# Kernel optimization log

Measured on AMD Instinct MI355X. Metric: run time of the kernel, lower is better.

Reference implementation:

```python
import jax, jax.numpy as jnp
import numpy as np

N = 8192
IN_F = 512
OUT_F = 64
ALPHA = 0.2   # LeakyReLU negative slope
STDV = 0.2
NEG_INF = -9e15


def setup_inputs() -> dict:
    key = jax.random.key(0)
    k1, k2, k3, k4 = jax.random.split(key, 4)
    x = jax.random.normal(k1, (N, IN_F), dtype=jnp.float32)
    adj = jax.random.randint(k2, (N, N), 0, 2, dtype=jnp.int32)
    W = jax.random.normal(k3, (IN_F, OUT_F), dtype=jnp.float32) * STDV
    a = jax.random.normal(k4, (2 * OUT_F, 1), dtype=jnp.float32) * STDV
    return {"x": x, "adj": adj, "W": W, "a": a}


def reference(x, adj, W, a):
    # Wh: [N, F']
    Wh = x @ W
    # attention logits: e[i,j] = leakyrelu(Wh[i]@a1 + Wh[j]@a2)
    Wh1 = Wh @ a[:OUT_F, :]   # [N, 1]
    Wh2 = Wh @ a[OUT_F:, :]   # [N, 1]
    e = Wh1 + Wh2.T           # [N, N] via broadcast
    e = jnp.where(e >= 0, e, ALPHA * e)  # LeakyReLU
    # mask by adjacency, row softmax
    masked = jnp.where(adj > 0, e, jnp.float32(NEG_INF))
    attention = jax.nn.softmax(masked, axis=1)
    # dropout rate is 0.0 in this config -> identity
    h_prime = attention @ Wh  # [N, F']
    out = jnp.where(h_prime > 0, h_prime, jnp.expm1(h_prime))  # ELU
    return out, attention
```

## Files before the change

kernel.cpp:

```cpp
#include <hip/hip_runtime.h>
#include <cmath>

#define Nn    8192
#define INF_  512
#define OUTF  64

typedef __attribute__((ext_vector_type(4))) int   i4;
typedef __attribute__((ext_vector_type(4))) float f4v;
typedef __attribute__((ext_vector_type(8))) short s8;
typedef __attribute__((ext_vector_type(4))) float f32x4;
typedef unsigned long long u64;

__device__ __forceinline__ float lrelu(float v) { return fmaxf(v, 0.2f * v); }

__device__ __forceinline__ unsigned int f2bf(float f) {
    unsigned int u = __float_as_uint(f);
    u = (u + 0x7FFFu + ((u >> 16) & 1u)) >> 16;
    return u;
}

__global__ __launch_bounds__(1024, 8) void k1_wh(
    const float* __restrict__ x, const float* __restrict__ W,
    const float* __restrict__ a, unsigned short* __restrict__ WhT,
    float* __restrict__ Wh1, float* __restrict__ Wh2)
{
    __shared__ float part[3][16][64];
    __shared__ unsigned short stage[64][16];
    const int t    = threadIdx.x;
    const int s    = t >> 8;
    const int r    = (t >> 4) & 15;
    const int cg   = (t & 15) << 2;
    const int row0 = blockIdx.x * 16;
    const int row  = row0 + r;
    const float* __restrict__ xr = x + (size_t)row * INF_ + s * 128;
    const float* __restrict__ Wp = W + (size_t)s * 128 * OUTF;

    float4 acc = make_float4(0.f, 0.f, 0.f, 0.f);
    for (int k = 0; k < 128; k += 4) {
        const float4 xv = *(const float4*)(xr + k);
        const float* wp = Wp + (size_t)k * OUTF + cg;
        const float4 w0 = *(const float4*)(wp);
        const float4 w1 = *(const float4*)(wp + OUTF);
        const float4 w2 = *(const float4*)(wp + 2 * OUTF);
        const float4 w3 = *(const float4*)(wp + 3 * OUTF);
        acc.x += xv.x * w0.x + xv.y * w1.x + xv.z * w2.x + xv.w * w3.x;
        acc.y += xv.x * w0.y + xv.y * w1.y + xv.z * w2.y + xv.w * w3.y;
        acc.z += xv.x * w0.z + xv.y * w1.z + xv.z * w2.z + xv.w * w3.z;
        acc.w += xv.x * w0.w + xv.y * w1.w + xv.z * w2.w + xv.w * w3.w;
    }
    if (s > 0) *(float4*)&part[s - 1][r][cg] = acc;
    __syncthreads();
    if (s == 0) {
        const float4 pa = *(const float4*)&part[0][r][cg];
        const float4 pb = *(const float4*)&part[1][r][cg];
        const float4 pc = *(const float4*)&part[2][r][cg];
        acc.x += pa.x + pb.x + pc.x;
        acc.y += pa.y + pb.y + pc.y;
        acc.z += pa.z + pb.z + pc.z;
        acc.w += pa.w + pb.w + pc.w;
        stage[cg + 0][r] = (unsigned short)f2bf(acc.x);
        stage[cg + 1][r] = (unsigned short)f2bf(acc.y);
        stage[cg + 2][r] = (unsigned short)f2bf(acc.z);
        stage[cg + 3][r] = (unsigned short)f2bf(acc.w);

        float p1 = acc.x * a[cg]        + acc.y * a[cg + 1]
                 + acc.z * a[cg + 2]    + acc.w * a[cg + 3];
        float p2 = acc.x * a[OUTF + cg]     + acc.y * a[OUTF + cg + 1]
                 + acc.z * a[OUTF + cg + 2] + acc.w * a[OUTF + cg + 3];
        #pragma unroll
        for (int off = 8; off; off >>= 1) {
            p1 += __shfl_xor(p1, off);
            p2 += __shfl_xor(p2, off);
        }
        if ((t & 15) == 0) { Wh1[row] = p1; Wh2[row] = p2; }
    }
    __syncthreads();
    if (t < 256) {
        const int col = t >> 2;
        const int q   = t & 3;
        const u64 v = *(const u64*)&stage[col][q * 4];
        *(u64*)(WhT + (size_t)col * Nn + row0 + q * 4) = v;
    }
}

__global__ __launch_bounds__(1024, 8) void k2_fused(
    const int* __restrict__ adj, const unsigned short* __restrict__ WhT,
    const float* __restrict__ Wh1, const float* __restrict__ Wh2,
    float* __restrict__ outp, float* __restrict__ att)
{
    __shared__ alignas(16) unsigned short att_t[2][16 * 256];
    __shared__ float red[3][4][16][16];

    const int t    = threadIdx.x;
    const int lane = t & 63;
    const int w    = t >> 6;
    const int row0 = blockIdx.x * 16;
    const int row  = row0 + w;
    const int* __restrict__ adjrow = adj + (size_t)row * Nn;
    const float h1 = Wh1[row];

    u64 mk0 = 0, mk1 = 0;
    float S = 0.f;
    {
        i4 av[4];
        #pragma unroll
        for (int i = 0; i < 4; ++i)
            av[i] = *((const i4*)(adjrow + 256 * i) + lane);
        #pragma unroll
        for (int i = 0; i < 32; ++i) {
            const i4 a = av[i & 3];
            if (i < 28)
                av[i & 3] = *((const i4*)(adjrow + 256 * (i + 4)) + lane);
            const f4v w4 = *((const f4v*)(Wh2 + 256 * i) + lane);
            const int nib = (a.x != 0 ? 1 : 0) | (a.y != 0 ? 2 : 0)
                          | (a.z != 0 ? 4 : 0) | (a.w != 0 ? 8 : 0);
            S += (nib & 1) ? __expf(lrelu(h1 + w4.x)) : 0.f;
            S += (nib & 2) ? __expf(lrelu(h1 + w4.y)) : 0.f;
            S += (nib & 4) ? __expf(lrelu(h1 + w4.z)) : 0.f;
            S += (nib & 8) ? __expf(lrelu(h1 + w4.w)) : 0.f;
            if (i < 16) mk0 |= (u64)nib << (i * 4);
            else        mk1 |= (u64)nib << ((i - 16) * 4);
        }
    }
    #pragma unroll
    for (int off = 32; off; off >>= 1) S += __shfl_xor(S, off);
    const float is = 1.0f / S;

    const int ct = w & 3;
    const int kq = w >> 2;
    f32x4 acc = {0.f, 0.f, 0.f, 0.f};

    auto produce = [&](int c, int bf) {
        const int jb = c * 256;
        const f4v w2 = *((const f4v*)(Wh2 + jb) + lane);
        const int nib = (int)(((c & 16) ? mk1 : mk0) >> ((c & 15) * 4)) & 15;
        const float v0 = (nib & 1) ? __expf(lrelu(h1 + w2.x)) * is : 0.f;
        const float v1 = (nib & 2) ? __expf(lrelu(h1 + w2.y)) * is : 0.f;
        const float v2 = (nib & 4) ? __expf(lrelu(h1 + w2.z)) * is : 0.f;
        const float v3 = (nib & 8) ? __expf(lrelu(h1 + w2.w)) * is : 0.f;
        f4v st; st.x = v0; st.y = v1; st.z = v2; st.w = v3;
        __builtin_nontemporal_store(st, (f4v*)(att + (size_t)row * Nn + jb) + lane);
        const u64 pk = (u64)(f2bf(v0) | (f2bf(v1) << 16))
                     | ((u64)(f2bf(v2) | (f2bf(v3) << 16)) << 32);
        int byte = w * 512 + lane * 8;  byte ^= (w & 7) << 4;
        *(u64*)((char*)att_t[bf] + byte) = pk;
    };

    const int ar = lane & 15;
    const int ag = lane >> 4;
    auto bload = [&](int c, int ss) -> s8 {
        const int ks = kq * 2 + ss;
        return *(const s8*)(WhT + (size_t)(ct * 16 + ar) * Nn
                            + c * 256 + ks * 32 + ag * 8);
    };
    auto amfma = [&](int bf, s8 b0, s8 b1) {
        #pragma unroll
        for (int ss = 0; ss < 2; ++ss) {
            const int ks = kq * 2 + ss;
            int byte = ar * 512 + ks * 64 + ag * 16;
            byte ^= (ar & 7) << 4;
            const s8 af = *(const s8*)((char*)att_t[bf] + byte);
            acc = __builtin_amdgcn_mfma_f32_16x16x32_bf16(af, ss ? b1 : b0, acc, 0, 0, 0);
        }
    };

    s8 b0 = bload(0, 0), b1 = bload(0, 1);
    produce(0, 0);
    asm volatile("s_waitcnt lgkmcnt(0)" ::: "memory");
    __builtin_amdgcn_s_barrier();
    for (int c = 0; c < Nn / 256 - 1; ++c) {
        produce(c + 1, (c + 1) & 1);
        const s8 nb0 = bload(c + 1, 0);
        const s8 nb1 = bload(c + 1, 1);
        amfma(c & 1, b0, b1);
        asm volatile("s_waitcnt lgkmcnt(0)" ::: "memory");
        __builtin_amdgcn_s_barrier();
        b0 = nb0; b1 = nb1;
    }
    amfma((Nn / 256 - 1) & 1, b0, b1);

    __syncthreads();
    if (kq > 0) {
        #pragma unroll
        for (int q = 0; q < 4; ++q) red[kq - 1][ct][ag * 4 + q][ar] = acc[q];
    }
    __syncthreads();
    if (kq == 0) {
        #pragma unroll
        for (int q = 0; q < 4; ++q) {
            const int r = ag * 4 + q;
            float v = acc[q] + red[0][ct][r][ar] + red[1][ct][r][ar] + red[2][ct][r][ar];
            v = v > 0.f ? v : expm1f(v);
            outp[(size_t)(row0 + r) * OUTF + ct * 16 + ar] = v;
        }
    }
}

extern "C" void kernel_launch(void* const* d_in, const int* in_sizes, int n_in,
                              void* d_out, int out_size, void* d_ws, size_t ws_size,
                              hipStream_t stream)
{
    const float* x   = (const float*)d_in[0];
    const int*   adj = (const int*)d_in[1];
    const float* W   = (const float*)d_in[2];
    const float* a   = (const float*)d_in[3];

    float* outp = (float*)d_out;
    float* att  = outp + (size_t)Nn * OUTF;

    float* Wh1 = (float*)d_ws;
    float* Wh2 = Wh1 + Nn;
    unsigned short* WhT = (unsigned short*)(Wh2 + Nn);

    hipLaunchKernelGGL(k1_wh,    dim3(Nn / 16), dim3(1024), 0, stream,
                       x, W, a, WhT, Wh1, Wh2);
    hipLaunchKernelGGL(k2_fused, dim3(Nn / 16), dim3(1024), 0, stream,
                       adj, WhT, Wh1, Wh2, outp, att);
}
```

Before: 179.0 us.

## Stage x tile in LDS and block-cooperatively stream adjacency into shared bitmask

In k1, the 16x512 x tile is loaded cooperatively into shared memory with nontemporal loads, and the GEMV reads x from LDS instead of per-thread global reads. In k2, the whole block streams 16 adjacency rows contiguously (each thread covers 4 columns across all rows) instead of one wave per row. Neighbor masks go into an 8-bit-per-nibble LDS bitmask, and the per-row softmax denominators are reduced across waves through shared memory. The aim is more coalesced, longer streaming access to the dominant 256MB adj read. The cost is extra LDS (32KB bitmask), extra barriers, and a one-ahead prefetch instead of four.

Measured after the change: 162.0 us. -9.5%, faster.

```diff
diff --git a/kernel.cpp b/kernel.cpp
--- a/kernel.cpp
+++ b/kernel.cpp
@@ -24,20 +24,30 @@
     const float* __restrict__ a, unsigned short* __restrict__ WhT,
     float* __restrict__ Wh1, float* __restrict__ Wh2)
 {
+    __shared__ float xs[16][520];
     __shared__ float part[3][16][64];
     __shared__ unsigned short stage[64][16];
     const int t    = threadIdx.x;
+    const int row0 = blockIdx.x * 16;
+
+    #pragma unroll
+    for (int s2 = 0; s2 < 2; ++s2) {
+        const int idx = s2 * 4096 + 4 * t;
+        const f4v v = __builtin_nontemporal_load(
+            (const f4v*)(x + (size_t)row0 * INF_ + idx));
+        *(f4v*)&xs[idx >> 9][idx & 511] = v;
+    }
+    __syncthreads();
+
     const int s    = t >> 8;
     const int r    = (t >> 4) & 15;
     const int cg   = (t & 15) << 2;
-    const int row0 = blockIdx.x * 16;
     const int row  = row0 + r;
-    const float* __restrict__ xr = x + (size_t)row * INF_ + s * 128;
     const float* __restrict__ Wp = W + (size_t)s * 128 * OUTF;
 
     float4 acc = make_float4(0.f, 0.f, 0.f, 0.f);
     for (int k = 0; k < 128; k += 4) {
-        const float4 xv = *(const float4*)(xr + k);
+        const float4 xv = *(const float4*)&xs[r][s * 128 + k];
         const float* wp = Wp + (size_t)k * OUTF + cg;
         const float4 w0 = *(const float4*)(wp);
         const float4 w1 = *(const float4*)(wp + OUTF);
@@ -88,43 +98,61 @@
     const float* __restrict__ Wh1, const float* __restrict__ Wh2,
     float* __restrict__ outp, float* __restrict__ att)
 {
+    __shared__ unsigned char bm8[16][2048];
     __shared__ alignas(16) unsigned short att_t[2][16 * 256];
     __shared__ float red[3][4][16][16];
+    __shared__ float sm_Sp[16][16];
+    __shared__ float sm_is[16];
 
     const int t    = threadIdx.x;
     const int lane = t & 63;
     const int w    = t >> 6;
     const int row0 = blockIdx.x * 16;
-    const int row  = row0 + w;
-    const int* __restrict__ adjrow = adj + (size_t)row * Nn;
+
+    {
+        const i4* __restrict__ asrc = (const i4*)(adj + (size_t)row0 * Nn);
+        const int j0 = 4 * t;
+        const f4v w4a = *(const f4v*)(Wh2 + j0);
+        const f4v w4b = *(const f4v*)(Wh2 + 4096 + j0);
+        float Sp = 0.f;
+        i4 av = __builtin_nontemporal_load(asrc + t);
+        #pragma unroll
+        for (int s = 0; s < 32; ++s) {
+            const int r = s >> 1, h = s & 1;
+            i4 nxt;
+            if (s < 31)
+                nxt = __builtin_nontemporal_load(asrc + (s + 1) * 1024 + t);
+            const f4v w4 = h ? w4b : w4a;
+            const float h1r = Wh1[row0 + r];
+            const int nib = (av.x != 0 ? 1 : 0) | (av.y != 0 ? 2 : 0)
+                          | (av.z != 0 ? 4 : 0) | (av.w != 0 ? 8 : 0);
+            Sp += (nib & 1) ? __expf(lrelu(h1r + w4.x)) : 0.f;
+            Sp += (nib & 2) ? __expf(lrelu(h1r + w4.y)) : 0.f;
+            Sp += (nib & 4) ? __expf(lrelu(h1r + w4.z)) : 0.f;
+            Sp += (nib & 8) ? __expf(lrelu(h1r + w4.w)) : 0.f;
+            bm8[r][h * 1024 + t] = (unsigned char)nib;
+            if (h) {
+                #pragma unroll
+                for (int off = 32; off; off >>= 1) Sp += __shfl_xor(Sp, off);
+                if (lane == 0) sm_Sp[r][w] = Sp;
+                Sp = 0.f;
+            }
+            av = nxt;
+        }
+    }
+    __syncthreads();
+
+    {
+        float sv = sm_Sp[w][lane & 15];
+        #pragma unroll
+        for (int off = 8; off; off >>= 1) sv += __shfl_xor(sv, off);
+        if (lane == 0) sm_is[w] = 1.0f / sv;
+    }
+    __syncthreads();
+
+    const int row = row0 + w;
     const float h1 = Wh1[row];
-
-    u64 mk0 = 0, mk1 = 0;
-    float S = 0.f;
-    {
-        i4 av[4];
-        #pragma unroll
-        for (int i = 0; i < 4; ++i)
-            av[i] = *((const i4*)(adjrow + 256 * i) + lane);
-        #pragma unroll
-        for (int i = 0; i < 32; ++i) {
-            const i4 a = av[i & 3];
-            if (i < 28)
-                av[i & 3] = *((const i4*)(adjrow + 256 * (i + 4)) + lane);
-            const f4v w4 = *((const f4v*)(Wh2 + 256 * i) + lane);
-            const int nib = (a.x != 0 ? 1 : 0) | (a.y != 0 ? 2 : 0)
-                          | (a.z != 0 ? 4 : 0) | (a.w != 0 ? 8 : 0);
-            S += (nib & 1) ? __expf(lrelu(h1 + w4.x)) : 0.f;
-            S += (nib & 2) ? __expf(lrelu(h1 + w4.y)) : 0.f;
-            S += (nib & 4) ? __expf(lrelu(h1 + w4.z)) : 0.f;
-            S += (nib & 8) ? __expf(lrelu(h1 + w4.w)) : 0.f;
-            if (i < 16) mk0 |= (u64)nib << (i * 4);
-            else        mk1 |= (u64)nib << ((i - 16) * 4);
-        }
-    }
-    #pragma unroll
-    for (int off = 32; off; off >>= 1) S += __shfl_xor(S, off);
-    const float is = 1.0f / S;
+    const float is = sm_is[w];
 
     const int ct = w & 3;
     const int kq = w >> 2;
@@ -133,7 +161,7 @@
     auto produce = [&](int c, int bf) {
         const int jb = c * 256;
         const f4v w2 = *((const f4v*)(Wh2 + jb) + lane);
-        const int nib = (int)(((c & 16) ? mk1 : mk0) >> ((c & 15) * 4)) & 15;
+        const int nib = bm8[w][c * 64 + lane];
         const float v0 = (nib & 1) ? __expf(lrelu(h1 + w2.x)) * is : 0.f;
         const float v1 = (nib & 2) ? __expf(lrelu(h1 + w2.y)) * is : 0.f;
         const float v2 = (nib & 4) ? __expf(lrelu(h1 + w2.z)) * is : 0.f;
```
